# Kernel optimization log

Hardware: AMD Instinct MI355X
Metric: run time of the kernel (lower is better)

Reference implementation:

```python
import jax, jax.numpy as jnp
import numpy as np

STRIDE = 16
RATIOS = (0.5, 1.0, 2.0)
SCALES = (8, 16, 32)
NMS_THRESH = 0.7
NUM_PRE = 12000
NUM_POST = 2000
MIN_SIZE = 16.0


def _all_anchors(feat_h, feat_w):
    # base anchors centered at (stride/2, stride/2), (y1, x1, y2, x2)
    base = []
    for r in RATIOS:
        for s in SCALES:
            h = STRIDE * s * np.sqrt(r)
            w = STRIDE * s * np.sqrt(1.0 / r)
            c = STRIDE / 2.0
            base.append([c - h / 2.0, c - w / 2.0, c + h / 2.0, c + w / 2.0])
    base = np.asarray(base, np.float32)  # (A, 4)
    ys = np.arange(feat_h, dtype=np.float32) * STRIDE
    xs = np.arange(feat_w, dtype=np.float32) * STRIDE
    shift = np.stack(np.meshgrid(ys, xs, indexing='ij'), axis=-1)  # (H, W, 2) = (y, x)
    shift4 = np.concatenate([shift, shift], axis=-1)  # (H, W, 4)
    anchors = shift4[:, :, None, :] + base[None, None, :, :]  # (H, W, A, 4)
    return jnp.asarray(anchors.reshape(-1, 4))


def _conv(x, w, b, padding):
    y = jax.lax.conv_general_dilated(x, w, (1, 1), padding,
                                     dimension_numbers=('NCHW', 'OIHW', 'NCHW'))
    return y + b[None, :, None, None]


def _create_rpn_proposals(locs, scores, anchors, img_h, img_w):
    # box deparameterize (y1,x1,y2,x2 anchors; dy,dx,dh,dw locs)
    ha = anchors[:, 2] - anchors[:, 0]
    wa = anchors[:, 3] - anchors[:, 1]
    cya = anchors[:, 0] + 0.5 * ha
    cxa = anchors[:, 1] + 0.5 * wa
    cy = locs[:, 0] * ha + cya
    cx = locs[:, 1] * wa + cxa
    h = ha * jnp.exp(locs[:, 2])
    w = wa * jnp.exp(locs[:, 3])
    boxes = jnp.stack([cy - 0.5 * h, cx - 0.5 * w, cy + 0.5 * h, cx + 0.5 * w], axis=1)

    order = jnp.argsort(-scores)[:NUM_PRE]
    boxes = boxes[order]
    s = scores[order]

    lim = jnp.array([img_h, img_w, img_h, img_w], dtype=boxes.dtype)
    boxes = jnp.clip(boxes, 0.0, lim)
    valid = ((boxes[:, 2] - boxes[:, 0]) >= MIN_SIZE) & ((boxes[:, 3] - boxes[:, 1]) >= MIN_SIZE)

    areas = (boxes[:, 2] - boxes[:, 0]) * (boxes[:, 3] - boxes[:, 1])
    n = boxes.shape[0]
    idx = jnp.arange(n)

    def body(i, suppressed):
        bi = boxes[i]
        yy1 = jnp.maximum(bi[0], boxes[:, 0])
        xx1 = jnp.maximum(bi[1], boxes[:, 1])
        yy2 = jnp.minimum(bi[2], boxes[:, 2])
        xx2 = jnp.minimum(bi[3], boxes[:, 3])
        inter = jnp.maximum(yy2 - yy1, 0.0) * jnp.maximum(xx2 - xx1, 0.0)
        iou = inter / (areas[i] + areas - inter + 1e-10)
        new_sup = suppressed | ((iou > NMS_THRESH) & (idx > i))
        return jnp.where(suppressed[i], suppressed, new_sup)

    suppressed = jax.lax.fori_loop(0, n, body, ~valid)
    keep = (~suppressed) & valid
    rank = jnp.cumsum(keep) - 1
    tgt = jnp.where(keep & (rank < NUM_POST), rank, NUM_POST)  # overflow slot
    out = jnp.zeros((NUM_POST + 1, 4), boxes.dtype).at[tgt].set(boxes)[:NUM_POST]
    return out  # (2000, 4), zero-padded if fewer kept


def setup_inputs() -> dict:
    key = jax.random.key(0)
    ks = jax.random.split(key, 7)
    in_c, out_c, A = 1024, 512, 9
    x = jax.random.normal(ks[0], (1, in_c, 64, 64), dtype=jnp.float32)
    conv_w = jax.random.normal(ks[1], (out_c, in_c, 3, 3), jnp.float32) * 0.01
    conv_b = jnp.zeros((out_c,), jnp.float32)
    score_w = jax.random.normal(ks[2], (A * 2, out_c, 1, 1), jnp.float32) * 0.01
    score_b = jnp.zeros((A * 2,), jnp.float32)
    loc_w = jax.random.normal(ks[3], (A * 4, out_c, 1, 1), jnp.float32) * 0.01
    loc_b = jnp.zeros((A * 4,), jnp.float32)
    return {"x": x, "conv_w": conv_w, "conv_b": conv_b,
            "score_w": score_w, "score_b": score_b,
            "loc_w": loc_w, "loc_b": loc_b,
            "img_h": 1024, "img_w": 1024}


def reference(x, conv_w, conv_b, score_w, score_b, loc_w, loc_b, img_h, img_w):
    _, _, fh, fw = x.shape
    anchors = _all_anchors(fh, fw)  # (fh*fw*A, 4)
    h = jax.nn.leaky_relu(_conv(x, conv_w, conv_b, 'SAME'), 0.01)
    rpn_locs = _conv(h, loc_w, loc_b, 'VALID').transpose(0, 2, 3, 1).reshape(-1, 4)
    rpn_scores = _conv(h, score_w, score_b, 'VALID').transpose(0, 2, 3, 1).reshape(-1, 2)
    fg = jax.nn.softmax(rpn_scores, axis=1)[:, 1]
    rois = _create_rpn_proposals(jax.lax.stop_gradient(rpn_locs),
                                 jax.lax.stop_gradient(fg),
                                 anchors, img_h, img_w)
    return rpn_locs, rpn_scores, rois, anchors
```

## Files before the change

kernel.cpp:

```cpp
#include <hip/hip_runtime.h>
#include <cstdint>
#include <cstddef>
#include <math.h>

#define NANCH    36864
#define NPRE     12000
#define NPRE_PAD 12032
#define NW       188
#define SORT_N   16384
#define NPOST    2000

__device__ __forceinline__ int tribase(int ci) { return ci * NW - (ci * (ci - 1)) / 2; }

__global__ __launch_bounds__(256, 2)
void k_conv_ks(const float* __restrict__ xg, const float* __restrict__ wg_,
               double* __restrict__ p0g, double* __restrict__ p1g)
{
    __shared__ float wlds[144 * 64];
    __shared__ float xlds[16 * 4 * 76];
    const int tid = threadIdx.x;
    const int ks  = blockIdx.x >> 8;
    const int inner = blockIdx.x & 255;
    const int oct = inner & 7;
    const int rp  = inner >> 3;
    const int oc0 = oct << 6;
    const int y0  = rp << 1;
    const int ocg = tid >> 4;
    const int pxg = tid & 15;
    const int ry  = pxg >> 3;
    const int cx0 = (pxg & 7) << 3;
    const int lane = tid & 63, wv = tid >> 6;
    const int icbase = ks << 9;

    double acc[4][8];
#pragma unroll
    for (int o = 0; o < 4; ++o)
#pragma unroll
        for (int j = 0; j < 8; ++j) acc[o][j] = 0.0;

    int xoff[17], loff[17];
#pragma unroll
    for (int t = 0; t < 17; ++t) {
        int f = tid + 256 * t;
        if (f < 4224) {
            int ic = f / 264; int r = f - ic * 264; int srow = r / 66; int gc = r - srow * 66;
            loff[t] = (ic * 4 + srow) * 76 + gc;
            int gy = y0 + srow - 1, gx = gc - 1;
            xoff[t] = (gy >= 0 && gy < 64 && gx >= 0 && gx < 64)
                      ? (ic * 4096 + gy * 64 + gx) : -1;
        } else { loff[t] = -1; xoff[t] = -1; }
    }

    const float* wbase = wg_ + (size_t)(oc0 + lane) * 9216 + (size_t)icbase * 9 + wv;
    const float* xbase = xg + (size_t)icbase * 4096;
    float wreg[36], xreg[17];

#pragma unroll
    for (int t = 0; t < 36; ++t) wreg[t] = wbase[4 * t];
#pragma unroll
    for (int t = 0; t < 17; ++t) xreg[t] = (xoff[t] >= 0) ? xbase[xoff[t]] : 0.f;

    for (int kc = 0; kc < 32; ++kc) {
        __syncthreads();
#pragma unroll
        for (int t = 0; t < 36; ++t) wlds[(wv + 4 * t) * 64 + lane] = wreg[t];
#pragma unroll
        for (int t = 0; t < 17; ++t)
            if (loff[t] >= 0) xlds[loff[t]] = xreg[t];
        if (kc < 31) {
            const float* wp = wbase + (kc + 1) * 144;
            const float* xp = xbase + (size_t)(kc + 1) * 16 * 4096;
#pragma unroll
            for (int t = 0; t < 36; ++t) wreg[t] = wp[4 * t];
#pragma unroll
            for (int t = 0; t < 17; ++t) xreg[t] = (xoff[t] >= 0) ? xp[xoff[t]] : 0.f;
        }
        __syncthreads();
#pragma unroll 1
        for (int ic = 0; ic < 16; ++ic) {
#pragma unroll
            for (int ky = 0; ky < 3; ++ky) {
                const float* xr = &xlds[(ic * 4 + ry + ky) * 76 + cx0];
                float4 t0 = *(const float4*)(xr);
                float4 t1 = *(const float4*)(xr + 4);
                float2 t2 = *(const float2*)(xr + 8);
                double xwd[10] = {t0.x, t0.y, t0.z, t0.w, t1.x, t1.y, t1.z, t1.w, t2.x, t2.y};
#pragma unroll
                for (int kx = 0; kx < 3; ++kx) {
                    const float4 wq = *(const float4*)&wlds[(ic * 9 + ky * 3 + kx) * 64 + (ocg << 2)];
                    double wdv[4] = {wq.x, wq.y, wq.z, wq.w};
#pragma unroll
                    for (int o = 0; o < 4; ++o)
#pragma unroll
                        for (int j = 0; j < 8; ++j)
                            acc[o][j] = fma(wdv[o], xwd[j + kx], acc[o][j]);
                }
            }
        }
    }
    double* pg = ks ? p1g : p0g;
#pragma unroll
    for (int o = 0; o < 4; ++o) {
        const int oc = oc0 + (ocg << 2) + o;
        double* pp = pg + (size_t)oc * 4096 + (y0 + ry) * 64 + cx0;
#pragma unroll
        for (int j = 0; j < 8; j += 2)
            *(double2*)(pp + j) = make_double2(acc[o][j], acc[o][j + 1]);
    }
}

__global__ __launch_bounds__(256, 4)
void k_comb(const double* __restrict__ p0, const double* __restrict__ p1,
            const float* __restrict__ bg, float* __restrict__ hg)
{
    int i2 = (blockIdx.x * 256 + threadIdx.x) * 2;
    double2 a = *(const double2*)(p0 + i2);
    double2 b = *(const double2*)(p1 + i2);
    double bo = (double)bg[i2 >> 12];
    double t0 = a.x + b.x + bo, t1 = a.y + b.y + bo;
    float v0 = (float)((t0 >= 0.0) ? t0 : 0.01 * t0);
    float v1 = (float)((t1 >= 0.0) ? t1 : 0.01 * t1);
    *(float2*)(hg + i2) = make_float2(v0, v1);
}

__global__ __launch_bounds__(256, 1)
void k_conv_full(const float* __restrict__ xg, const float* __restrict__ wg_,
                 const float* __restrict__ bg, float* __restrict__ hg)
{
    __shared__ float wlds[144 * 64];
    __shared__ float xlds[16 * 4 * 76];
    const int tid = threadIdx.x;
    const int oct = blockIdx.x & 7;
    const int rp  = blockIdx.x >> 3;
    const int oc0 = oct << 6;
    const int y0  = rp << 1;
    const int ocg = tid >> 4;
    const int pxg = tid & 15;
    const int ry  = pxg >> 3;
    const int cx0 = (pxg & 7) << 3;
    const int lane = tid & 63, wv = tid >> 6;
    double acc[4][8];
#pragma unroll
    for (int o = 0; o < 4; ++o)
#pragma unroll
        for (int j = 0; j < 8; ++j) acc[o][j] = 0.0;
    int xoff[17], loff[17];
#pragma unroll
    for (int t = 0; t < 17; ++t) {
        int f = tid + 256 * t;
        if (f < 4224) {
            int ic = f / 264; int r = f - ic * 264; int srow = r / 66; int gc = r - srow * 66;
            loff[t] = (ic * 4 + srow) * 76 + gc;
            int gy = y0 + srow - 1, gx = gc - 1;
            xoff[t] = (gy >= 0 && gy < 64 && gx >= 0 && gx < 64)
                      ? (ic * 4096 + gy * 64 + gx) : -1;
        } else { loff[t] = -1; xoff[t] = -1; }
    }
    const float* wbase = wg_ + (size_t)(oc0 + lane) * 9216 + wv;
    float wreg[36], xreg[17];
#pragma unroll
    for (int t = 0; t < 36; ++t) wreg[t] = wbase[4 * t];
#pragma unroll
    for (int t = 0; t < 17; ++t) xreg[t] = (xoff[t] >= 0) ? xg[xoff[t]] : 0.f;
    for (int kc = 0; kc < 64; ++kc) {
        __syncthreads();
#pragma unroll
        for (int t = 0; t < 36; ++t) wlds[(wv + 4 * t) * 64 + lane] = wreg[t];
#pragma unroll
        for (int t = 0; t < 17; ++t)
            if (loff[t] >= 0) xlds[loff[t]] = xreg[t];
        if (kc < 63) {
            const float* wp = wbase + (kc + 1) * 144;
            const float* xp = xg + (size_t)(kc + 1) * 16 * 4096;
#pragma unroll
            for (int t = 0; t < 36; ++t) wreg[t] = wp[4 * t];
#pragma unroll
            for (int t = 0; t < 17; ++t) xreg[t] = (xoff[t] >= 0) ? xp[xoff[t]] : 0.f;
        }
        __syncthreads();
#pragma unroll 1
        for (int ic = 0; ic < 16; ++ic) {
#pragma unroll
            for (int ky = 0; ky < 3; ++ky) {
                const float* xr = &xlds[(ic * 4 + ry + ky) * 76 + cx0];
                float4 t0 = *(const float4*)(xr);
                float4 t1 = *(const float4*)(xr + 4);
                float2 t2 = *(const float2*)(xr + 8);
                double xwd[10] = {t0.x, t0.y, t0.z, t0.w, t1.x, t1.y, t1.z, t1.w, t2.x, t2.y};
#pragma unroll
                for (int kx = 0; kx < 3; ++kx) {
                    const float4 wq = *(const float4*)&wlds[(ic * 9 + ky * 3 + kx) * 64 + (ocg << 2)];
                    double wdv[4] = {wq.x, wq.y, wq.z, wq.w};
#pragma unroll
                    for (int o = 0; o < 4; ++o)
#pragma unroll
                        for (int j = 0; j < 8; ++j)
                            acc[o][j] = fma(wdv[o], xwd[j + kx], acc[o][j]);
                }
            }
        }
    }
#pragma unroll
    for (int o = 0; o < 4; ++o) {
        const int oc = oc0 + (ocg << 2) + o;
        const double bo = (double)bg[oc];
        float* hp = hg + (size_t)oc * 4096 + (y0 + ry) * 64 + cx0;
        float v[8];
#pragma unroll
        for (int j = 0; j < 8; ++j) {
            double t = acc[o][j] + bo;
            v[j] = (float)((t >= 0.0) ? t : 0.01 * t);
        }
        *(float4*)(hp)     = make_float4(v[0], v[1], v[2], v[3]);
        *(float4*)(hp + 4) = make_float4(v[4], v[5], v[6], v[7]);
    }
}

__global__ __launch_bounds__(256, 1)
void k_heads(const float* __restrict__ hg, const float* __restrict__ loc_w,
             const float* __restrict__ loc_b, const float* __restrict__ score_w,
             const float* __restrict__ score_b, const int* __restrict__ imh,
             const int* __restrict__ imw, float* __restrict__ out,
             float* __restrict__ boxes_all, unsigned long long* __restrict__ keys64)
{
    __shared__ float  hch[64 * 64];
    __shared__ float  wch[54 * 64];
    __shared__ float  ol[54 * 64];
    __shared__ double sld[18 * 64];
    const int y = blockIdx.x, tid = threadIdx.x;
    const int px = tid & 63, cg = tid >> 6;
    double acc[14];
#pragma unroll
    for (int u = 0; u < 14; ++u) acc[u] = 0.0;
    for (int cc = 0; cc < 8; ++cc) {
        __syncthreads();
#pragma unroll
        for (int t = 0; t < 16; ++t) {
            int f = tid + 256 * t;
            hch[f] = hg[(size_t)(cc * 64 + (f >> 6)) * 4096 + y * 64 + (f & 63)];
        }
#pragma unroll
        for (int t = 0; t < 14; ++t) {
            int f = tid + 256 * t;
            if (f < 54 * 64) {
                int ch = f >> 6, c = f & 63;
                wch[f] = (ch < 36) ? loc_w[ch * 512 + cc * 64 + c]
                                   : score_w[(ch - 36) * 512 + cc * 64 + c];
            }
        }
        __syncthreads();
        for (int c = 0; c < 64; ++c) {
            double hvd = (double)hch[c * 64 + px];
#pragma unroll
            for (int u = 0; u < 14; ++u) {
                int ch = cg + 4 * u;
                if (ch < 54) acc[u] = fma((double)wch[ch * 64 + c], hvd, acc[u]);
            }
        }
    }
    __syncthreads();
#pragma unroll
    for (int u = 0; u < 14; ++u) {
        int ch = cg + 4 * u;
        if (ch < 54) {
            double s = acc[u] + (double)((ch < 36) ? loc_b[ch] : score_b[ch - 36]);
            ol[ch * 64 + px] = (float)s;
            if (ch >= 36) sld[(ch - 36) * 64 + px] = s;
        }
    }
    __syncthreads();
    for (int f = tid; f < 64 * 36; f += 256) {
        int p = f / 36, ch = f - 36 * p;
        out[(size_t)(y * 64 + p) * 36 + ch] = ol[ch * 64 + p];
    }
    for (int f = tid; f < 64 * 18; f += 256) {
        int p = f / 18, ch = f - 18 * p;
        out[147456 + (size_t)(y * 64 + p) * 18 + ch] = ol[(36 + ch) * 64 + p];
    }
    const float fy = (float)(*imh), fx = (float)(*imw);
    float* anch = out + 229184;
    for (int t2 = tid; t2 < 576; t2 += 256) {
        int p = t2 / 9, a = t2 - 9 * p;
        int pg = y * 64 + p;
        int ar = a / 3, as = a - 3 * ar;
        double rr = (ar == 0) ? 0.5 : ((ar == 1) ? 1.0 : 2.0);
        double ss = (as == 0) ? 8.0 : ((as == 1) ? 16.0 : 32.0);
        double hh = 16.0 * ss * sqrt(rr), wwd = 16.0 * ss * sqrt(1.0 / rr);
        float by1 = (float)(8.0 - hh * 0.5), bx1 = (float)(8.0 - wwd * 0.5);
        float by2 = (float)(8.0 + hh * 0.5), bx2 = (float)(8.0 + wwd * 0.5);
        float sy = (float)(y * 16), sx = (float)(p * 16);
        float a0 = sy + by1, a1 = sx + bx1, a2 = sy + by2, a3 = sx + bx2;
        int base = (pg * 9 + a) * 4;
        anch[base + 0] = a0; anch[base + 1] = a1; anch[base + 2] = a2; anch[base + 3] = a3;
        double d = sld[(a * 2 + 1) * 64 + p] - sld[(a * 2) * 64 + p];
        long long bits = __double_as_longlong(d);
        unsigned long long u64 =
            (unsigned long long)(bits ^ ((bits >> 63) | (long long)0x8000000000000000LL));
        unsigned long long v = ~u64;
        keys64[pg * 9 + a] = (v & 0xFFFFFFFFFFFF0000ULL) | (unsigned long long)(pg * 9 + a);
        float dy = ol[(a * 4 + 0) * 64 + p], dxv = ol[(a * 4 + 1) * 64 + p];
        float dh = ol[(a * 4 + 2) * 64 + p], dwv = ol[(a * 4 + 3) * 64 + p];
        float hA = a2 - a0, wA = a3 - a1;
        float cya = a0 + 0.5f * hA, cxa = a1 + 0.5f * wA;
        float cy = dy * hA + cya, cx = dxv * wA + cxa;
        float hb = hA * expf(dh), wb = wA * expf(dwv);
        float b0 = fminf(fmaxf(cy - 0.5f * hb, 0.f), fy);
        float b1 = fminf(fmaxf(cx - 0.5f * wb, 0.f), fx);
        float b2 = fminf(fmaxf(cy + 0.5f * hb, 0.f), fy);
        float b3 = fminf(fmaxf(cx + 0.5f * wb, 0.f), fx);
        boxes_all[base + 0] = b0; boxes_all[base + 1] = b1;
        boxes_all[base + 2] = b2; boxes_all[base + 3] = b3;
    }
}

__global__ __launch_bounds__(1024, 1)
void k_select(const unsigned long long* __restrict__ keys64,
              const float* __restrict__ boxes_all,
              unsigned long long* __restrict__ sortbuf, float* __restrict__ sbox,
              float* __restrict__ areas, unsigned long long* __restrict__ suppr)
{
    __shared__ unsigned int hist[256];
    __shared__ unsigned int sh_below, sh_prefix, sh_nsel;
    __shared__ unsigned long long tile[4096];
    const int tid = threadIdx.x;
    if (tid == 0) { sh_below = 0; sh_prefix = 0; sh_nsel = 0; }
    __syncthreads();
    for (int p = 3; p >= 0; --p) {
        if (tid < 256) hist[tid] = 0;
        __syncthreads();
        unsigned int pref = sh_prefix;
        int shift = p * 8;
        for (int i = tid; i < NANCH; i += 1024) {
            unsigned int k = (unsigned int)(keys64[i] >> 32);
            bool match = (p == 3) || ((k >> (shift + 8)) == pref);
            if (match) atomicAdd(&hist[(k >> shift) & 255u], 1u);
        }
        __syncthreads();
        if (tid == 0) {
            unsigned int below = sh_below, cacc = 0;
            int b = 0;
            for (; b < 256; ++b) {
                if (below + cacc + hist[b] >= NPRE) break;
                cacc += hist[b];
            }
            if (b > 255) b = 255;
            sh_below = below + cacc;
            sh_prefix = (pref << 8) | (unsigned int)b;
        }
        __syncthreads();
    }
    const unsigned int P = sh_prefix;
    for (int i = tid; i < NANCH; i += 1024) {
        unsigned long long k = keys64[i];
        if ((unsigned int)(k >> 32) <= P) {
            unsigned int pos = atomicAdd(&sh_nsel, 1u);
            if (pos < SORT_N) sortbuf[pos] = k;
        }
    }
    __syncthreads();
    unsigned int nsel = sh_nsel; if (nsel > SORT_N) nsel = SORT_N;
    for (unsigned int i = nsel + tid; i < SORT_N; i += 1024) sortbuf[i] = ~0ULL;
    __syncthreads();
    for (int T = 0; T < 4; ++T) {
        for (int t = tid; t < 4096; t += 1024) tile[t] = sortbuf[T * 4096 + t];
        __syncthreads();
        for (int k2 = 2; k2 <= 4096; k2 <<= 1) {
            for (int j = k2 >> 1; j > 0; j >>= 1) {
                for (int t = tid; t < 2048; t += 1024) {
                    int i = ((t & ~(j - 1)) << 1) | (t & (j - 1));
                    int ip = i | j;
                    bool up = (((T * 4096 + i) & k2) == 0);
                    unsigned long long A = tile[i], B = tile[ip];
                    if ((A > B) == up) { tile[i] = B; tile[ip] = A; }
                }
                __syncthreads();
            }
        }
        for (int t = tid; t < 4096; t += 1024) sortbuf[T * 4096 + t] = tile[t];
        __syncthreads();
    }
    auto gstage = [&](int k2, int j) {
        for (int t = tid; t < 8192; t += 1024) {
            int i = ((t & ~(j - 1)) << 1) | (t & (j - 1));
            int ip = i | j;
            bool up = ((i & k2) == 0);
            unsigned long long A = sortbuf[i], B = sortbuf[ip];
            if ((A > B) == up) { sortbuf[i] = B; sortbuf[ip] = A; }
        }
        __syncthreads();
    };
    auto ltail = [&](int k2) {
        for (int T = 0; T < 4; ++T) {
            for (int t = tid; t < 4096; t += 1024) tile[t] = sortbuf[T * 4096 + t];
            __syncthreads();
            for (int j = 2048; j > 0; j >>= 1) {
                for (int t = tid; t < 2048; t += 1024) {
                    int i = ((t & ~(j - 1)) << 1) | (t & (j - 1));
                    int ip = i | j;
                    bool up = (((T * 4096 + i) & k2) == 0);
                    unsigned long long A = tile[i], B = tile[ip];
                    if ((A > B) == up) { tile[i] = B; tile[ip] = A; }
                }
                __syncthreads();
            }
            for (int t = tid; t < 4096; t += 1024) sortbuf[T * 4096 + t] = tile[t];
            __syncthreads();
        }
    };
    gstage(8192, 4096);  ltail(8192);
    gstage(16384, 8192); gstage(16384, 4096); ltail(16384);

    if (tid < NW) suppr[tid] = (tid == NW - 1) ? 0xFFFFFFFF00000000ULL : 0ULL;
    __syncthreads();
    for (int r = tid; r < NPRE_PAD; r += 1024) {
        float b0 = 0, b1 = 0, b2 = 0, b3 = 0;
        if (r < NPRE) {
            unsigned int idx = (unsigned int)(sortbuf[r] & 0xFFFFULL);
            const float* bp = boxes_all + (size_t)idx * 4;
            b0 = bp[0]; b1 = bp[1]; b2 = bp[2]; b3 = bp[3];
        }
        sbox[r * 4 + 0] = b0; sbox[r * 4 + 1] = b1;
        sbox[r * 4 + 2] = b2; sbox[r * 4 + 3] = b3;
        areas[r] = (b2 - b0) * (b3 - b1);
        if (r < NPRE) {
            bool valid = ((b2 - b0) >= 16.0f) && ((b3 - b1) >= 16.0f);
            if (!valid) atomicOr(&suppr[r >> 6], 1ULL << (r & 63));
        }
    }
}

__global__ __launch_bounds__(256, 1)
void k_mask(const float* __restrict__ sbox, const float* __restrict__ areas,
            unsigned long long* __restrict__ mask)
{
    const int cj = blockIdx.x, q = blockIdx.y;
    __shared__ float4 bx[64];
    __shared__ float aj[64];
    const int t = threadIdx.x;
    const int j0 = cj * 64;
    if (t < 64) { bx[t] = ((const float4*)sbox)[j0 + t]; aj[t] = areas[j0 + t]; }
    __syncthreads();
    const int c0 = ((cj + 1) * q) >> 2, c1 = ((cj + 1) * (q + 1)) >> 2;
    for (int i0 = c0 * 64; i0 < c1 * 64; i0 += 256) {
        int i = i0 + t;
        if (i < c1 * 64) {
            const float4 p = ((const float4*)sbox)[i];
            const float ai = areas[i];
            unsigned long long w = 0;
            for (int jj = 0; jj < 64; ++jj) {
                float4 qb = bx[jj];
                float yy1 = fmaxf(p.x, qb.x), xx1 = fmaxf(p.y, qb.y);
                float yy2 = fminf(p.z, qb.z), xx2 = fminf(p.w, qb.w);
                float inter = fmaxf(yy2 - yy1, 0.f) * fmaxf(xx2 - xx1, 0.f);
                float iou = inter / (ai + aj[jj] - inter + 1e-10f);
                w |= ((unsigned long long)((iou > 0.7f) && (j0 + jj > i))) << jj;
            }
            int ci = i >> 6;
            mask[(size_t)(tribase(ci) + (cj - ci)) * 64 + (i & 63)] = w;
        }
    }
}

__global__ __launch_bounds__(256, 1)
void k_scan(const unsigned long long* __restrict__ mask,
            const unsigned long long* __restrict__ suppr,
            const float* __restrict__ sbox, float* __restrict__ rois)
{
    __shared__ unsigned long long rvs[NW];
    __shared__ unsigned long long curw;
    __shared__ unsigned long long keptw[NW];
    __shared__ int totkept, brk;
    __shared__ int pref[NW + 1];
    const int tid = threadIdx.x;
    if (tid < NW) { rvs[tid] = suppr[tid]; keptw[tid] = 0ULL; }
    if (tid == 0) { totkept = 0; brk = 0; }
    __syncthreads();
    for (int c = 0; c < NW; ++c) {
        if (tid < 64) {
            unsigned long long diag = mask[(size_t)tribase(c) * 64 + tid];
            unsigned long long w = rvs[c];
            for (int b = 0; b < 64; ++b) {
                unsigned long long db = __shfl(diag, b, 64);
                if (!((w >> b) & 1ULL)) w |= db;
            }
            if (tid == 0) {
                curw = w;
                keptw[c] = ~w;
                totkept += __popcll(~w);
                if (totkept >= NPOST) brk = 1;
            }
        }
        __syncthreads();
        if (brk) break;
        unsigned long long kw = ~curw;
        if (tid > c && tid < NW) {
            const unsigned long long* mrow = mask + (size_t)(tribase(c) + (tid - c)) * 64;
            unsigned long long a0 = 0, a1 = 0, a2 = 0, a3 = 0;
            for (int b = 0; b < 64; b += 4) {
                unsigned long long m0 = mrow[b + 0];
                unsigned long long m1 = mrow[b + 1];
                unsigned long long m2 = mrow[b + 2];
                unsigned long long m3 = mrow[b + 3];
                if ((kw >> (b + 0)) & 1ULL) a0 |= m0;
                if ((kw >> (b + 1)) & 1ULL) a1 |= m1;
                if ((kw >> (b + 2)) & 1ULL) a2 |= m2;
                if ((kw >> (b + 3)) & 1ULL) a3 |= m3;
            }
            rvs[tid] |= a0 | a1 | a2 | a3;
        }
        __syncthreads();
    }
    __syncthreads();
    if (tid == 0) {
        int s = 0;
        for (int c = 0; c < NW; ++c) { pref[c] = s; s += __popcll(keptw[c]); }
        pref[NW] = s;
    }
    __syncthreads();
    int total = pref[NW]; if (total > NPOST) total = NPOST;
    for (int r = total * 4 + tid; r < NPOST * 4; r += 256) rois[r] = 0.f;
    if (tid < NW) {
        unsigned long long kw = keptw[tid];
        int r = pref[tid];
        for (int b = 0; b < 64; ++b) {
            if ((kw >> b) & 1ULL) {
                if (r < NPOST) {
                    const float* bp = sbox + (size_t)(tid * 64 + b) * 4;
                    rois[r * 4 + 0] = bp[0]; rois[r * 4 + 1] = bp[1];
                    rois[r * 4 + 2] = bp[2]; rois[r * 4 + 3] = bp[3];
                }
                ++r;
            }
        }
    }
}

extern "C" void kernel_launch(void* const* d_in, const int* in_sizes, int n_in,
                              void* d_out, int out_size, void* d_ws, size_t ws_size,
                              hipStream_t stream)
{
    const float* x       = (const float*)d_in[0];
    const float* conv_w  = (const float*)d_in[1];
    const float* conv_b  = (const float*)d_in[2];
    const float* score_w = (const float*)d_in[3];
    const float* score_b = (const float*)d_in[4];
    const float* loc_w   = (const float*)d_in[5];
    const float* loc_b   = (const float*)d_in[6];
    const int*   imh     = (const int*)d_in[7];
    const int*   imw     = (const int*)d_in[8];
    float* out = (float*)d_out;
    char* ws = (char*)d_ws;
    float* h                    = (float*)(ws);
    double* P0                  = (double*)(ws + 8388608);
    double* P1                  = (double*)(ws + 25165824);
    float* boxes_all            = (float*)(ws + 8388608);
    unsigned long long* keys64  = (unsigned long long*)(ws + 8978432);
    float* sbox                 = (float*)(ws + 9273344);
    float* areas                = (float*)(ws + 9465856);
    unsigned long long* suppr   = (unsigned long long*)(ws + 9513984);
    unsigned long long* sortbuf = (unsigned long long*)(ws + 9515520);
    unsigned long long* mask    = (unsigned long long*)(ws + 9646592);

    if (ws_size >= 41943040) {
        k_conv_ks<<<512, 256, 0, stream>>>(x, conv_w, P0, P1);
        k_comb   <<<4096, 256, 0, stream>>>(P0, P1, conv_b, h);
    } else {
        k_conv_full<<<256, 256, 0, stream>>>(x, conv_w, conv_b, h);
    }
    k_heads <<<64, 256, 0, stream>>>(h, loc_w, loc_b, score_w, score_b, imh, imw,
                                     out, boxes_all, keys64);
    k_select<<<1, 1024, 0, stream>>>(keys64, boxes_all, sortbuf, sbox, areas, suppr);
    k_mask  <<<dim3(188, 4), 256, 0, stream>>>(sbox, areas, mask);
    k_scan  <<<1, 256, 0, stream>>>(mask, suppr, sbox, out + 221184);
}
```

Baseline: 1.861 ms.

## Store NMS mask densely for coalesced scan reads and split heads kernel

The suppression mask moves from a packed triangular layout to a dense [box][column-word] layout. In the serial scan, adjacent threads now read adjacent words, so loads coalesce, and the row-OR is skipped when no box in the current word was kept. Separately, k_heads splits each feature row across four blocks, giving 256 blocks instead of 64 for more parallelism. In exchange the mask roughly doubles in workspace size, and each k_heads block reloads the full weight tile.

```diff
diff --git a/kernel.cpp b/kernel.cpp
--- a/kernel.cpp
+++ b/kernel.cpp
@@ -9,8 +9,6 @@
 #define NW       188
 #define SORT_N   16384
 #define NPOST    2000
-
-__device__ __forceinline__ int tribase(int ci) { return ci * NW - (ci * (ci - 1)) / 2; }
 
 __global__ __launch_bounds__(256, 2)
 void k_conv_ks(const float* __restrict__ xg, const float* __restrict__ wg_,
@@ -223,21 +221,23 @@
              const int* __restrict__ imw, float* __restrict__ out,
              float* __restrict__ boxes_all, unsigned long long* __restrict__ keys64)
 {
-    __shared__ float  hch[64 * 64];
+    __shared__ float  hch[64 * 16];
     __shared__ float  wch[54 * 64];
-    __shared__ float  ol[54 * 64];
-    __shared__ double sld[18 * 64];
-    const int y = blockIdx.x, tid = threadIdx.x;
-    const int px = tid & 63, cg = tid >> 6;
-    double acc[14];
-#pragma unroll
-    for (int u = 0; u < 14; ++u) acc[u] = 0.0;
+    __shared__ float  ol[54 * 16];
+    __shared__ double sld[18 * 16];
+    const int y = blockIdx.x >> 2, q = blockIdx.x & 3, px0 = q << 4;
+    const int tid = threadIdx.x;
+    const int px = tid & 15, cg = tid >> 4;
+    double acc[4];
+#pragma unroll
+    for (int u = 0; u < 4; ++u) acc[u] = 0.0;
+
     for (int cc = 0; cc < 8; ++cc) {
         __syncthreads();
 #pragma unroll
-        for (int t = 0; t < 16; ++t) {
+        for (int t = 0; t < 4; ++t) {
             int f = tid + 256 * t;
-            hch[f] = hg[(size_t)(cc * 64 + (f >> 6)) * 4096 + y * 64 + (f & 63)];
+            hch[f] = hg[(size_t)(cc * 64 + (f >> 4)) * 4096 + y * 64 + px0 + (f & 15)];
         }
 #pragma unroll
         for (int t = 0; t < 14; ++t) {
@@ -250,56 +250,56 @@
         }
         __syncthreads();
         for (int c = 0; c < 64; ++c) {
-            double hvd = (double)hch[c * 64 + px];
-#pragma unroll
-            for (int u = 0; u < 14; ++u) {
-                int ch = cg + 4 * u;
+            double hvd = (double)hch[c * 16 + px];
+#pragma unroll
+            for (int u = 0; u < 4; ++u) {
+                int ch = cg + 16 * u;
                 if (ch < 54) acc[u] = fma((double)wch[ch * 64 + c], hvd, acc[u]);
             }
         }
     }
     __syncthreads();
 #pragma unroll
-    for (int u = 0; u < 14; ++u) {
-        int ch = cg + 4 * u;
+    for (int u = 0; u < 4; ++u) {
+        int ch = cg + 16 * u;
         if (ch < 54) {
             double s = acc[u] + (double)((ch < 36) ? loc_b[ch] : score_b[ch - 36]);
-            ol[ch * 64 + px] = (float)s;
-            if (ch >= 36) sld[(ch - 36) * 64 + px] = s;
-        }
-    }
-    __syncthreads();
-    for (int f = tid; f < 64 * 36; f += 256) {
+            ol[ch * 16 + px] = (float)s;
+            if (ch >= 36) sld[(ch - 36) * 16 + px] = s;
+        }
+    }
+    __syncthreads();
+    for (int f = tid; f < 16 * 36; f += 256) {
         int p = f / 36, ch = f - 36 * p;
-        out[(size_t)(y * 64 + p) * 36 + ch] = ol[ch * 64 + p];
-    }
-    for (int f = tid; f < 64 * 18; f += 256) {
+        out[(size_t)(y * 64 + px0 + p) * 36 + ch] = ol[ch * 16 + p];
+    }
+    for (int f = tid; f < 16 * 18; f += 256) {
         int p = f / 18, ch = f - 18 * p;
-        out[147456 + (size_t)(y * 64 + p) * 18 + ch] = ol[(36 + ch) * 64 + p];
+        out[147456 + (size_t)(y * 64 + px0 + p) * 18 + ch] = ol[(36 + ch) * 16 + p];
     }
     const float fy = (float)(*imh), fx = (float)(*imw);
     float* anch = out + 229184;
-    for (int t2 = tid; t2 < 576; t2 += 256) {
+    for (int t2 = tid; t2 < 144; t2 += 256) {
         int p = t2 / 9, a = t2 - 9 * p;
-        int pg = y * 64 + p;
+        int pg = y * 64 + px0 + p;
         int ar = a / 3, as = a - 3 * ar;
         double rr = (ar == 0) ? 0.5 : ((ar == 1) ? 1.0 : 2.0);
         double ss = (as == 0) ? 8.0 : ((as == 1) ? 16.0 : 32.0);
         double hh = 16.0 * ss * sqrt(rr), wwd = 16.0 * ss * sqrt(1.0 / rr);
         float by1 = (float)(8.0 - hh * 0.5), bx1 = (float)(8.0 - wwd * 0.5);
         float by2 = (float)(8.0 + hh * 0.5), bx2 = (float)(8.0 + wwd * 0.5);
-        float sy = (float)(y * 16), sx = (float)(p * 16);
+        float sy = (float)(y * 16), sx = (float)((px0 + p) * 16);
         float a0 = sy + by1, a1 = sx + bx1, a2 = sy + by2, a3 = sx + bx2;
         int base = (pg * 9 + a) * 4;
         anch[base + 0] = a0; anch[base + 1] = a1; anch[base + 2] = a2; anch[base + 3] = a3;
-        double d = sld[(a * 2 + 1) * 64 + p] - sld[(a * 2) * 64 + p];
+        double d = sld[(a * 2 + 1) * 16 + p] - sld[(a * 2) * 16 + p];
         long long bits = __double_as_longlong(d);
         unsigned long long u64 =
             (unsigned long long)(bits ^ ((bits >> 63) | (long long)0x8000000000000000LL));
         unsigned long long v = ~u64;
         keys64[pg * 9 + a] = (v & 0xFFFFFFFFFFFF0000ULL) | (unsigned long long)(pg * 9 + a);
-        float dy = ol[(a * 4 + 0) * 64 + p], dxv = ol[(a * 4 + 1) * 64 + p];
-        float dh = ol[(a * 4 + 2) * 64 + p], dwv = ol[(a * 4 + 3) * 64 + p];
+        float dy = ol[(a * 4 + 0) * 16 + p], dxv = ol[(a * 4 + 1) * 16 + p];
+        float dh = ol[(a * 4 + 2) * 16 + p], dwv = ol[(a * 4 + 3) * 16 + p];
         float hA = a2 - a0, wA = a3 - a1;
         float cya = a0 + 0.5f * hA, cxa = a1 + 0.5f * wA;
         float cy = dy * hA + cya, cx = dxv * wA + cxa;
@@ -455,8 +455,7 @@
                 float iou = inter / (ai + aj[jj] - inter + 1e-10f);
                 w |= ((unsigned long long)((iou > 0.7f) && (j0 + jj > i))) << jj;
             }
-            int ci = i >> 6;
-            mask[(size_t)(tribase(ci) + (cj - ci)) * 64 + (i & 63)] = w;
+            mask[(size_t)i * NW + cj] = w;
         }
     }
 }
@@ -477,7 +476,7 @@
     __syncthreads();
     for (int c = 0; c < NW; ++c) {
         if (tid < 64) {
-            unsigned long long diag = mask[(size_t)tribase(c) * 64 + tid];
+            unsigned long long diag = mask[(size_t)(c * 64 + tid) * NW + c];
             unsigned long long w = rvs[c];
             for (int b = 0; b < 64; ++b) {
                 unsigned long long db = __shfl(diag, b, 64);
@@ -493,20 +492,15 @@
         __syncthreads();
         if (brk) break;
         unsigned long long kw = ~curw;
-        if (tid > c && tid < NW) {
-            const unsigned long long* mrow = mask + (size_t)(tribase(c) + (tid - c)) * 64;
-            unsigned long long a0 = 0, a1 = 0, a2 = 0, a3 = 0;
-            for (int b = 0; b < 64; b += 4) {
-                unsigned long long m0 = mrow[b + 0];
-                unsigned long long m1 = mrow[b + 1];
-                unsigned long long m2 = mrow[b + 2];
-                unsigned long long m3 = mrow[b + 3];
-                if ((kw >> (b + 0)) & 1ULL) a0 |= m0;
-                if ((kw >> (b + 1)) & 1ULL) a1 |= m1;
-                if ((kw >> (b + 2)) & 1ULL) a2 |= m2;
-                if ((kw >> (b + 3)) & 1ULL) a3 |= m3;
-            }
-            rvs[tid] |= a0 | a1 | a2 | a3;
+        if (kw && tid > c && tid < NW) {
+            const unsigned long long* mbase = mask + (size_t)(c * 64) * NW + tid;
+            unsigned long long a0 = 0;
+#pragma unroll 8
+            for (int b = 0; b < 64; ++b) {
+                unsigned long long m = mbase[(size_t)b * NW];
+                if ((kw >> b) & 1ULL) a0 |= m;
+            }
+            rvs[tid] |= a0;
         }
         __syncthreads();
     }
@@ -567,8 +561,8 @@
     } else {
         k_conv_full<<<256, 256, 0, stream>>>(x, conv_w, conv_b, h);
     }
-    k_heads <<<64, 256, 0, stream>>>(h, loc_w, loc_b, score_w, score_b, imh, imw,
-                                     out, boxes_all, keys64);
+    k_heads <<<256, 256, 0, stream>>>(h, loc_w, loc_b, score_w, score_b, imh, imw,
+                                      out, boxes_all, keys64);
     k_select<<<1, 1024, 0, stream>>>(keys64, boxes_all, sortbuf, sbox, areas, suppr);
     k_mask  <<<dim3(188, 4), 256, 0, stream>>>(sbox, areas, mask);
     k_scan  <<<1, 256, 0, stream>>>(mask, suppr, sbox, out + 221184);
```

Result: slower. 2.173 ms (+16.8%).
